# Kernel optimization log

Measured on AMD Instinct MI355X. Metric: run time of the kernel, lower is better.

## Reference

```python
import jax, jax.numpy as jnp
import numpy as np

WINDOW, STRIDE, BLUR_THR, EPS = 8, 4, 50.0, 1e-5
DN = ('NCHW', 'OIHW', 'NCHW')


def _conv(x, w, pad=0, stride=1):
    return jax.lax.conv_general_dilated(x, w, (stride, stride), [(pad, pad), (pad, pad)], dimension_numbers=DN)


def _detect_rgb_invalid(rgb):
    # Laplacian-variance blur detector: unfold(8,stride=4) -> var -> threshold -> scatter windows
    B, _, H, W = rgb.shape
    gray = 0.299 * rgb[:, 0] + 0.587 * rgb[:, 1] + 0.114 * rgb[:, 2]
    gray = jnp.clip(gray * 255.0, 0.0, 255.0)[:, None]  # [B,1,H,W]
    lap_k = jnp.array([[0., 1., 0.], [1., -4., 1.], [0., 1., 0.]], gray.dtype)[None, None]
    lap = _conv(gray, lap_k, pad=1)
    ones_k = jnp.ones((1, 1, WINDOW, WINDOW), gray.dtype)
    s1 = jax.lax.conv_general_dilated(lap, ones_k, (STRIDE, STRIDE), 'VALID', dimension_numbers=DN)
    s2 = jax.lax.conv_general_dilated(lap * lap, ones_k, (STRIDE, STRIDE), 'VALID', dimension_numbers=DN)
    n = float(WINDOW * WINDOW)
    var = (s2 - s1 * s1 / n) / (n - 1.0)  # unbiased var, matches torch.var
    flags = (var[:, 0] < BLUR_THR).astype(gray.dtype)  # [B, hs, ws]
    hs, ws = flags.shape[1], flags.shape[2]
    rep = jnp.repeat(jnp.repeat(flags, STRIDE, axis=1), STRIDE, axis=2)  # [B, hs*4, ws*4]
    mask = jnp.zeros((B, H, W), gray.dtype)
    # each 8x8 window covers 2x2 stride-cells -> max over the 4 shifted copies
    for dy in range(0, WINDOW, STRIDE):
        for dx in range(0, WINDOW, STRIDE):
            mask = mask.at[:, dy:dy + hs * STRIDE, dx:dx + ws * STRIDE].max(rep)
    return mask


def _bn_relu(x, g, b):
    m = x.mean((0, 2, 3), keepdims=True)
    v = x.var((0, 2, 3), keepdims=True)  # biased, matches BN training-mode normalization
    return jax.nn.relu(g[None, :, None, None] * (x - m) / jnp.sqrt(v + EPS) + b[None, :, None, None])


def _attend(main, aux, inv, ft_w, bn_g, bn_b, sa_w, ca1_w, ca2_w):
    B, C, H, W = main.shape
    aux_t = _bn_relu(_conv(aux, ft_w, pad=1), bn_g, bn_b)
    xs = jnp.broadcast_to(jnp.linspace(-1.0, 1.0, W, dtype=main.dtype)[None, None, None, :], (B, 1, H, W))
    ys = jnp.broadcast_to(jnp.linspace(-1.0, 1.0, H, dtype=main.dtype)[None, None, :, None], (B, 1, H, W))
    sp_in = jnp.concatenate([main.mean(1, keepdims=True), main.max(axis=1, keepdims=True), xs, ys], axis=1)
    sw = jax.nn.sigmoid(_conv(sp_in, sa_w, pad=3))  # [B,1,H,W]
    gap = main.mean((2, 3), keepdims=True)
    cw = jax.nn.sigmoid(_conv(jax.nn.relu(_conv(gap, ca1_w)), ca2_w))  # [B,C,1,1]
    return aux_t * sw * cw * (1.0 + inv[:, None])


def _compensate(main, aux, inv, params):
    # early-return when mask is all-zero in torch is mathematically identical to the blend
    comp = _attend(main, aux, inv, *params)
    m = inv[:, None]
    return main * (1.0 - m) + comp * m


def _down(mask, h, w):
    H, W = mask.shape[1], mask.shape[2]
    return mask[:, ::H // h, ::W // w]  # exact nearest-neighbor for integer ratios


def _forward(rgb_feat0, rgb_feat1, rgb_feat2, depth_feat0, depth_feat1, depth_feat2, rgb_img, depth_img,
             ft_w0, bn_g0, bn_b0, sa_w0, ca1_w0, ca2_w0,
             ft_w1, bn_g1, bn_b1, sa_w1, ca1_w1, ca2_w1,
             ft_w2, bn_g2, bn_b2, sa_w2, ca1_w2, ca2_w2):
    rgb_mask = _detect_rgb_invalid(rgb_img)
    depth_mask = (depth_img[:, 2] <= 0.0).astype(rgb_img.dtype)
    rgb_feats = (rgb_feat0, rgb_feat1, rgb_feat2)
    depth_feats = (depth_feat0, depth_feat1, depth_feat2)
    params = ((ft_w0, bn_g0, bn_b0, sa_w0, ca1_w0, ca2_w0),
              (ft_w1, bn_g1, bn_b1, sa_w1, ca1_w1, ca2_w1),
              (ft_w2, bn_g2, bn_b2, sa_w2, ca1_w2, ca2_w2))
    outs_r, outs_d = [], []
    for rf, df, p in zip(rgb_feats, depth_feats, params):
        h, w = rf.shape[2], rf.shape[3]
        ri = _down(rgb_mask, h, w)
        di = _down(depth_mask, h, w)
        outs_r.append(_compensate(rf, df, ri, p))
        outs_d.append(_compensate(df, rf, di, p))
    return tuple(outs_r) + tuple(outs_d)


def setup_inputs() -> dict:
    key = jax.random.key(0)
    ks = iter(jax.random.split(key, 40))
    B, H, W = 8, 512, 512
    chans = [256, 512, 1024]
    feat_hw = [(64, 64), (32, 32), (16, 16)]
    d = {}
    for i, (C, (fh, fw)) in enumerate(zip(chans, feat_hw)):
        d[f'rgb_feat{i}'] = jax.random.normal(next(ks), (B, C, fh, fw), jnp.float32)
        d[f'depth_feat{i}'] = jax.random.normal(next(ks), (B, C, fh, fw), jnp.float32)
    d['rgb_img'] = jax.random.uniform(next(ks), (B, 3, H, W), jnp.float32)
    d['depth_img'] = jax.random.normal(next(ks), (B, 3, H, W), jnp.float32)
    for i, C in enumerate(chans):
        r = C // 16
        d[f'ft_w{i}'] = jax.random.normal(next(ks), (C, C, 3, 3), jnp.float32) * 0.02
        d[f'bn_g{i}'] = jnp.ones((C,), jnp.float32)
        d[f'bn_b{i}'] = jnp.zeros((C,), jnp.float32)
        d[f'sa_w{i}'] = jax.random.normal(next(ks), (1, 4, 7, 7), jnp.float32) * 0.1
        d[f'ca1_w{i}'] = jax.random.normal(next(ks), (r, C, 1, 1), jnp.float32) * 0.1
        d[f'ca2_w{i}'] = jax.random.normal(next(ks), (C, r, 1, 1), jnp.float32) * 0.1
    return d


def reference(rgb_feat0, rgb_feat1, rgb_feat2, depth_feat0, depth_feat1, depth_feat2, rgb_img, depth_img,
              ft_w0, bn_g0, bn_b0, sa_w0, ca1_w0, ca2_w0,
              ft_w1, bn_g1, bn_b1, sa_w1, ca1_w1, ca2_w1,
              ft_w2, bn_g2, bn_b2, sa_w2, ca1_w2, ca2_w2):
    return _forward(rgb_feat0, rgb_feat1, rgb_feat2, depth_feat0, depth_feat1, depth_feat2, rgb_img, depth_img,
                    ft_w0, bn_g0, bn_b0, sa_w0, ca1_w0, ca2_w0,
                    ft_w1, bn_g1, bn_b1, sa_w1, ca1_w1, ca2_w1,
                    ft_w2, bn_g2, bn_b2, sa_w2, ca1_w2, ca2_w2)
```

## Files before the change

kernel.cpp:

```cpp
#include <hip/hip_runtime.h>
#include <math.h>

#define B8 8
typedef unsigned short ushort_t;
typedef __attribute__((ext_vector_type(8))) short bf16x8;
typedef __attribute__((ext_vector_type(4))) float f32x4;

static __device__ __forceinline__ float sigmoidf_(float x){ return 1.f/(1.f+expf(-x)); }

static __device__ __forceinline__ ushort_t f2bf(float f){
  unsigned u = __float_as_uint(f);
  u = u + 0x7fffu + ((u>>16)&1u);
  return (ushort_t)(u>>16);
}
static __device__ __forceinline__ float bflo(unsigned q){ return __uint_as_float(q << 16); }
static __device__ __forceinline__ float bfhi(unsigned q){ return __uint_as_float(q & 0xffff0000u); }

__device__ __forceinline__ void gload_lds16(const ushort_t* g, ushort_t* l){
  __builtin_amdgcn_global_load_lds((const __attribute__((address_space(1))) unsigned int*)(const void*)g,
                                   (__attribute__((address_space(3))) unsigned int*)(void*)l, 16, 0, 0);
}

__global__ __launch_bounds__(256) void k_flags2(const float* __restrict__ rgb,
                                                float* __restrict__ flags){
  __shared__ float sg[70][71];
  int bx = blockIdx.x & 7, by = (blockIdx.x >> 3) & 7, b = blockIdx.x >> 6;
  int wy0 = by*16, wx0 = bx*16;
  int y0 = 4*wy0 - 1, x0 = 4*wx0 - 1;
  const float* p = rgb + (size_t)b*3*262144;
  int tid = threadIdx.x;
  for (int i = tid; i < 70*70; i += 256){
    int r = i/70, cX = i%70;
    int y = y0 + r, x = x0 + cX;
    float v = 0.f;
    if (y>=0 && y<512 && x>=0 && x<512){
      int ii = y*512+x;
      v = 0.299f*p[ii] + 0.587f*p[ii+262144] + 0.114f*p[ii+524288];
      v = fminf(fmaxf(v*255.f, 0.f), 255.f);
    }
    sg[r][cX] = v;
  }
  __syncthreads();
  int wy = wy0 + (tid>>4), wx = wx0 + (tid&15);
  if (wy > 126 || wx > 126) return;
  int ry = 4*(tid>>4) + 1, rx = 4*(tid&15) + 1;
  float s1 = 0.f, s2 = 0.f;
  #pragma unroll
  for (int iy=0; iy<8; ++iy){
    int r = ry+iy;
    #pragma unroll
    for (int ix=0; ix<8; ++ix){
      int cX = rx+ix;
      float c = sg[r][cX];
      float lap = sg[r-1][cX] + sg[r+1][cX] + sg[r][cX-1] + sg[r][cX+1] - 4.f*c;
      s1 += lap; s2 += lap*lap;
    }
  }
  float var = (s2 - s1*s1*(1.f/64.f)) * (1.f/63.f);
  flags[(size_t)b*16129 + wy*127 + wx] = (var < 50.f) ? 1.f : 0.f;
}

__global__ void k_masks3(const float* __restrict__ flags, const float* __restrict__ depth,
                         float* __restrict__ ri0, float* __restrict__ di0,
                         float* __restrict__ ri1, float* __restrict__ di1,
                         float* __restrict__ ri2, float* __restrict__ di2){
  int idx = blockIdx.x*256 + threadIdx.x;
  const int n0 = 8*4096, n1 = 8*1024, n2 = 8*256;
  float* ri; float* di; int h, st, i2;
  if (idx < n0){ ri=ri0; di=di0; h=64; st=8;  i2=idx; }
  else if (idx < n0+n1){ ri=ri1; di=di1; h=32; st=16; i2=idx-n0; }
  else if (idx < n0+n1+n2){ ri=ri2; di=di2; h=16; st=32; i2=idx-n0-n1; }
  else return;
  int b = i2/(h*h), i = i2%(h*h);
  int y = (i/h)*st, x = (i%h)*st;
  const float* f = flags + (size_t)b*16129;
  int fy = y>>2, fx = x>>2;
  float v = f[fy*127+fx];
  if (y>0)         v = fmaxf(v, f[(fy-1)*127+fx]);
  if (x>0)         v = fmaxf(v, f[fy*127+fx-1]);
  if (y>0 && x>0)  v = fmaxf(v, f[(fy-1)*127+fx-1]);
  ri[i2] = v;
  const int IHW = 262144;
  di[i2] = (depth[(size_t)b*3*IHW + 2*IHW + (size_t)y*512 + x] <= 0.f) ? 1.f : 0.f;
}

template<int C>
__global__ __launch_bounds__(256) void k_wrd2(const float* __restrict__ w, ushort_t* __restrict__ outp){
  __shared__ float swp[9*C];
  int co = blockIdx.x, tid = threadIdx.x;
  const int n = 9*C;
  const float* src = w + (size_t)co*n;
  for (int i=tid;i<n;i+=256) swp[i]=src[i];
  __syncthreads();
  ushort_t* dst = outp + (size_t)co*n;
  for (int j=tid;j<n;j+=256){
    int cb  = j / 576;
    int rem = j - cb*576;
    int kq  = rem >> 6;
    int cin = rem & 63;
    dst[j] = f2bf(swp[(cb*64 + cin)*9 + kq]);
  }
}

template<int C, int H, int W>
__global__ __launch_bounds__(256) void k_prep(const float* __restrict__ rgbf,
                                              const float* __restrict__ depf,
                                              ushort_t* __restrict__ outp,
                                              float* __restrict__ gpart,
                                              float* __restrict__ pmean,
                                              float* __restrict__ pmax_){
  const int W2 = W+2, H2 = H+2, CB = C/64;
  const int NHSZ = B8*H2*W2*C;
  const int HW = H*W;
  __shared__ float st[64*66];
  __shared__ float red[4][64];
  int bi = blockIdx.x;
  int f  = bi & 1; bi >>= 1;
  int cb = bi % CB; bi /= CB;
  int yy = bi % H2;
  int b  = bi / H2;
  int tid = threadIdx.x;
  const float* in = (f==0) ? rgbf : depf;
  int ndir = f ^ 1;
  ushort_t* outrow = outp + (size_t)ndir*NHSZ + ((size_t)(b*H2 + yy)*W2)*C + cb*64;
  bool pad_row = (yy == 0) || (yy == H2-1);
  if (!pad_row){
    int y = yy-1;
    const float* src = in + ((size_t)(b*C + cb*64)*H + y)*W;
    for (int i=tid; i<64*W; i+=256){
      int c = i / W, x = i % W;
      st[x*66 + c] = src[(size_t)c*H*W + x];
    }
  }
  __syncthreads();
  for (int j=tid; j<W2*8; j+=256){
    int x = j >> 3, cc = (j & 7)*8;
    ushort_t tmp[8];
    if (pad_row || x == 0 || x == W2-1){
      #pragma unroll
      for (int q=0;q<8;++q) tmp[q]=0;
    } else {
      const float* sp = &st[(x-1)*66 + cc];
      float2 a0 = *(const float2*)(sp+0);
      float2 a1 = *(const float2*)(sp+2);
      float2 a2 = *(const float2*)(sp+4);
      float2 a3 = *(const float2*)(sp+6);
      tmp[0]=f2bf(a0.x); tmp[1]=f2bf(a0.y); tmp[2]=f2bf(a1.x); tmp[3]=f2bf(a1.y);
      tmp[4]=f2bf(a2.x); tmp[5]=f2bf(a2.y); tmp[6]=f2bf(a3.x); tmp[7]=f2bf(a3.y);
    }
    *(bf16x8*)&outrow[(size_t)x*C + cc] = *(bf16x8*)tmp;
  }
  if (pad_row) return;
  int y = yy - 1;
  {
    int c = tid & 63, quarter = tid >> 6;
    float s = 0.f;
    for (int x = quarter; x < W; x += 4) s += st[x*66 + c];
    red[quarter][c] = s;
  }
  if (tid < W*4){
    int x = tid >> 2, sl = tid & 3;
    float ps = 0.f, pmx = -INFINITY;
    #pragma unroll
    for (int k=0;k<16;++k){
      float v = st[x*66 + sl*16 + k];
      ps += v; pmx = fmaxf(pmx, v);
    }
    ps += __shfl_xor(ps, 1); pmx = fmaxf(pmx, __shfl_xor(pmx, 1));
    ps += __shfl_xor(ps, 2); pmx = fmaxf(pmx, __shfl_xor(pmx, 2));
    if (sl == 0){
      size_t po = ((size_t)f*CB + cb)*((size_t)B8*HW) + (size_t)b*HW + (size_t)y*W + x;
      pmean[po] = ps; pmax_[po] = pmx;
    }
  }
  __syncthreads();
  if (tid < 64){
    float t4 = red[0][tid]+red[1][tid]+red[2][tid]+red[3][tid];
    gpart[(((size_t)f*B8 + b)*H + y)*C + (size_t)cb*64 + tid] = t4;
  }
}

template<int C, int H, int W, int KS>
__global__ __launch_bounds__(512)
void k_gemm_conv(const ushort_t* __restrict__ Aw, const ushort_t* __restrict__ nh,
                 ushort_t* __restrict__ Gm){
  const int K9 = 9*C;
  const int HW = H*W;
  const int N  = B8*HW;
  const int H2 = H+2, W2 = W+2;
  const int NT_N = N/256, NT_M = C/256;
  const int KCT = 36;
  const int NHSZ = B8*H2*W2*C;
  __shared__ ushort_t sA[2][16384];
  __shared__ ushort_t sB[2][16384];
  int tid = threadIdx.x;

  const int nwg = 2*KS*NT_M*NT_N;
  const int MK  = 2*KS*NT_M;
  int bid = blockIdx.x;
  int swz = (bid & 7)*(nwg >> 3) + (bid >> 3);
  int mk  = swz % MK;
  int n_t = swz / MK;
  int m_t = mk % NT_M;
  int kz2 = mk / NT_M;
  int dir = kz2 / KS, kz = kz2 % KS;

  const ushort_t* nhd = nh + (size_t)dir*NHSZ;
  int m0 = m_t*256, n0 = n_t*256;
  int l = tid & 63, wv_id = tid >> 6;
  int wm = wv_id >> 2, wn = wv_id & 3;
  int lrow = l & 15, lq = l >> 4;
  int lx7 = lrow & 7;

  long long aoffA[2][2], boffB[2][2];
  #pragma unroll
  for (int h=0; h<2; ++h){
    #pragma unroll
    for (int j=0; j<2; ++j){
      int c = j*512 + tid;
      int lr = h*128 + (c>>3);
      int slot = c & 7;
      int lslot = slot ^ (lr & 7);
      int q_ = lr >> 6, wm_ = (lr>>5)&1, loc = lr & 31;
      int r = wm_*128 + q_*32 + loc;
      aoffA[h][j] = (long long)(m0 + r)*K9 + lslot*8;
      int nn = n0 + lr;
      int b_ = nn / HW, rhw = nn % HW;
      int y = rhw / W, x = rhw % W;
      boffB[h][j] = ((long long)(b_*H2 + y + 1)*W2 + (x + 1))*(long long)C + lslot*8;
    }
  }

#define STAGE_A(s_, h_, kc_) do{                                    \
    long long oK = (long long)(kc_) << 6;                           \
    ushort_t* d0 = &sA[s_][(h_)*8192 + tid*8];                      \
    gload_lds16(Aw + aoffA[h_][0] + oK, d0);                        \
    gload_lds16(Aw + aoffA[h_][1] + oK, d0 + 4096);                 \
  }while(0)
#define STAGE_B(s_, h_, kc_) do{                                    \
    int cb_ = (kc_)/9, kq_ = (kc_) - cb_*9;                         \
    long long dv = (long long)((kq_/3 - 1)*W2 + (kq_%3 - 1))*C + ((long long)cb_<<6); \
    ushort_t* d0 = &sB[s_][(h_)*8192 + tid*8];                      \
    gload_lds16(nhd + boffB[h_][0] + dv, d0);                       \
    gload_lds16(nhd + boffB[h_][1] + dv, d0 + 4096);                \
  }while(0)

  f32x4 acc[8][4];
  #pragma unroll
  for (int i=0;i<8;++i)
    #pragma unroll
    for (int j=0;j<4;++j) acc[i][j] = (f32x4){0.f,0.f,0.f,0.f};

  int kc0 = kz*KCT;

  STAGE_A(0,0,kc0);   STAGE_A(0,1,kc0);
  STAGE_B(0,0,kc0);   STAGE_B(0,1,kc0);
  STAGE_B(1,0,kc0+1); STAGE_B(1,1,kc0+1);
  STAGE_A(1,0,kc0+1);
  asm volatile("s_waitcnt vmcnt(6)" ::: "memory");
  __builtin_amdgcn_s_barrier();

  for (int t=0; t<KCT; ++t){
    int cur = t & 1, nxt = cur ^ 1;
    int kc = kc0 + t;
    bf16x8 bf[4][2], afA[2][2], afB[2][2];

    #pragma unroll
    for (int ni=0;ni<4;++ni)
      #pragma unroll
      for (int kk=0;kk<2;++kk)
        bf[ni][kk] = *(const bf16x8*)&sB[cur][(wn*64 + ni*16 + lrow)*64 + ((kk*4+lq)^lx7)*8];
    #pragma unroll
    for (int mi=0;mi<2;++mi)
      #pragma unroll
      for (int kk=0;kk<2;++kk)
        afA[mi][kk] = *(const bf16x8*)&sA[cur][(wm*32 + mi*16 + lrow)*64 + ((kk*4+lq)^lx7)*8];
    #pragma unroll
    for (int mi=0;mi<2;++mi)
      #pragma unroll
      for (int kk=0;kk<2;++kk)
        afB[mi][kk] = *(const bf16x8*)&sA[cur][(64 + wm*32 + mi*16 + lrow)*64 + ((kk*4+lq)^lx7)*8];
    if (t+1 < KCT) STAGE_A(nxt,1,kc+1);
    __builtin_amdgcn_s_setprio(1);
    #pragma unroll
    for (int kk=0;kk<2;++kk)
      #pragma unroll
      for (int mi=0;mi<2;++mi)
        #pragma unroll
        for (int ni=0;ni<4;++ni)
          acc[mi][ni] = __builtin_amdgcn_mfma_f32_16x16x32_bf16(afA[mi][kk], bf[ni][kk], acc[mi][ni], 0,0,0);
    __builtin_amdgcn_s_setprio(0);
    asm volatile("s_waitcnt lgkmcnt(0)" ::: "memory");
    __builtin_amdgcn_sched_barrier(0);
    __builtin_amdgcn_s_barrier();

    #pragma unroll
    for (int mi=0;mi<2;++mi)
      #pragma unroll
      for (int kk=0;kk<2;++kk)
        afA[mi][kk] = *(const bf16x8*)&sA[cur][(128 + wm*32 + mi*16 + lrow)*64 + ((kk*4+lq)^lx7)*8];
    if (t+2 < KCT) STAGE_B(cur,0,kc+2);
    __builtin_amdgcn_s_setprio(1);
    #pragma unroll
    for (int kk=0;kk<2;++kk)
      #pragma unroll
      for (int mi=0;mi<2;++mi)
        #pragma unroll
        for (int ni=0;ni<4;++ni)
          acc[2+mi][ni] = __builtin_amdgcn_mfma_f32_16x16x32_bf16(afB[mi][kk], bf[ni][kk], acc[2+mi][ni], 0,0,0);
    __builtin_amdgcn_s_setprio(0);

    #pragma unroll
    for (int mi=0;mi<2;++mi)
      #pragma unroll
      for (int kk=0;kk<2;++kk)
        afB[mi][kk] = *(const bf16x8*)&sA[cur][(192 + wm*32 + mi*16 + lrow)*64 + ((kk*4+lq)^lx7)*8];
    if (t+2 < KCT) STAGE_B(cur,1,kc+2);
    __builtin_amdgcn_s_setprio(1);
    #pragma unroll
    for (int kk=0;kk<2;++kk)
      #pragma unroll
      for (int mi=0;mi<2;++mi)
        #pragma unroll
        for (int ni=0;ni<4;++ni)
          acc[4+mi][ni] = __builtin_amdgcn_mfma_f32_16x16x32_bf16(afA[mi][kk], bf[ni][kk], acc[4+mi][ni], 0,0,0);
    __builtin_amdgcn_s_setprio(0);

    if (t+2 < KCT) STAGE_A(cur,0,kc+2);
    __builtin_amdgcn_s_setprio(1);
    #pragma unroll
    for (int kk=0;kk<2;++kk)
      #pragma unroll
      for (int mi=0;mi<2;++mi)
        #pragma unroll
        for (int ni=0;ni<4;++ni)
          acc[6+mi][ni] = __builtin_amdgcn_mfma_f32_16x16x32_bf16(afB[mi][kk], bf[ni][kk], acc[6+mi][ni], 0,0,0);
    __builtin_amdgcn_s_setprio(0);
    if (t+2 < KCT) { asm volatile("s_waitcnt vmcnt(6)" ::: "memory"); }
    else           { asm volatile("s_waitcnt vmcnt(0)" ::: "memory"); }
    __builtin_amdgcn_sched_barrier(0);
    __builtin_amdgcn_s_barrier();
  }
#undef STAGE_A
#undef STAGE_B

  ushort_t* po = Gm + (size_t)kz2*C*N;
  #pragma unroll
  for (int ai=0;ai<8;++ai)
    #pragma unroll
    for (int ni=0;ni<4;++ni)
      #pragma unroll
      for (int r=0;r<4;++r)
        po[(size_t)(m0 + wm*128 + ai*16 + lq*4 + r)*N + n0 + wn*64 + ni*16 + lrow] = f2bf(acc[ai][ni][r]);
}

__global__ void k_sgc(const float* __restrict__ pmean, const float* __restrict__ pmax_,
                      float* __restrict__ spmean, float* __restrict__ spmax,
                      int CG, int BHW, float invC){
  int dir = blockIdx.y;
  int p = blockIdx.x*256 + threadIdx.x;
  if (p >= BHW) return;
  const float* pm = pmean + (size_t)dir*CG*BHW;
  const float* px = pmax_ + (size_t)dir*CG*BHW;
  float s = 0.f, m = -INFINITY;
  for (int g=0; g<CG; ++g){
    s += pm[(size_t)g*BHW + p];
    m = fmaxf(m, px[(size_t)g*BHW + p]);
  }
  spmean[(size_t)dir*BHW + p] = s*invC;
  spmax [(size_t)dir*BHW + p] = m;
}

__global__ void k_sw(const float* __restrict__ spmean, const float* __restrict__ spmax,
                     const float* __restrict__ sa, float* __restrict__ sw,
                     int H, int W){
  __shared__ float s_sa[196];
  int tid = threadIdx.x;
  if (tid < 196) s_sa[tid] = sa[tid];
  __syncthreads();
  int HW = H*W;
  int dir = blockIdx.y;
  int gpos = blockIdx.x*256 + tid;
  if (gpos >= B8*HW) return;
  int b = gpos/HW, i = gpos%HW;
  int y = i/W, x = i%W;
  float inv_w = 2.f/(float)(W-1), inv_h = 2.f/(float)(H-1);
  const float* pm = spmean + (size_t)dir*B8*HW + (size_t)b*HW;
  const float* px = spmax  + (size_t)dir*B8*HW + (size_t)b*HW;
  float acc = 0.f;
  for (int ky=0;ky<7;++ky){
    int yy = y+ky-3;
    if (yy<0 || yy>=H) continue;
    float ysv = -1.f + yy*inv_h;
    for (int kx=0;kx<7;++kx){
      int xx = x+kx-3;
      if (xx<0 || xx>=W) continue;
      float xsv = -1.f + xx*inv_w;
      int kk = ky*7+kx;
      acc += s_sa[kk]*pm[yy*W+xx] + s_sa[49+kk]*px[yy*W+xx]
           + s_sa[98+kk]*xsv + s_sa[147+kk]*ysv;
    }
  }
  sw[(size_t)dir*B8*HW + gpos] = sigmoidf_(acc);
}

__global__ void k_mlp(const float* __restrict__ gpart, const float* __restrict__ w1,
                      const float* __restrict__ w2, float* __restrict__ cw,
                      int C, int R, int SPLIT, float invHW){
  int b = blockIdx.x, dir = blockIdx.y;
  int tid = threadIdx.x;
  __shared__ float sg[1024];
  __shared__ float sh[64];
  const float* gp = gpart + (((size_t)dir*B8 + b)*SPLIT)*C;
  for (int c=tid;c<C;c+=256){
    float s = 0.f;
    for (int sp=0; sp<SPLIT; ++sp) s += gp[(size_t)sp*C + c];
    sg[c] = s*invHW;
  }
  __syncthreads();
  int r = tid>>2, q = tid&3;
  if (r < R){
    float s = 0.f;
    for (int c=q;c<C;c+=4) s += w1[(size_t)r*C + c]*sg[c];
    s += __shfl_xor(s,1); s += __shfl_xor(s,2);
    if (q==0) sh[r] = fmaxf(s, 0.f);
  }
  __syncthreads();
  for (int c2=tid; c2<C; c2+=256){
    float s = 0.f;
    for (int rr=0;rr<R;++rr) s += w2[(size_t)c2*R + rr]*sh[rr];
    cw[(size_t)dir*B8*C + (size_t)b*C + c2] = sigmoidf_(s);
  }
}

__global__ __launch_bounds__(256)
void k_bnfinal(const float* __restrict__ rgbf, const float* __restrict__ depf,
               const ushort_t* __restrict__ G,
               const float* __restrict__ g, const float* __restrict__ bb,
               const float* __restrict__ swp, const float* __restrict__ cwp,
               const float* __restrict__ ri, const float* __restrict__ di,
               float* __restrict__ out_r, float* __restrict__ out_d,
               int C, int HW, int hwShift, int ks){
  extern __shared__ char bnf_smem[];
  int c = blockIdx.x, dir = blockIdx.y, tid = threadIdx.x;
  int N = B8*HW;
  size_t MN = (size_t)C*N;
  const ushort_t* p0 = G + (size_t)dir*ks*MN + (size_t)c*N;
  const float* main_ = (dir==0) ? rgbf : depf;
  const float* mask  = (dir==0) ? ri : di;
  float* out = (dir==0) ? out_r : out_d;

  float s1 = 0.f, s2 = 0.f;
  if (ks == 1){
    uint4* cache = (uint4*)bnf_smem;
    for (int i = tid*8; i < N; i += 2048){
      uint4 q = *(const uint4*)(p0 + i);
      cache[i>>3] = q;
      float v0=bflo(q.x), v1=bfhi(q.x), v2=bflo(q.y), v3=bfhi(q.y);
      float v4=bflo(q.z), v5=bfhi(q.z), v6=bflo(q.w), v7=bfhi(q.w);
      s1 += v0+v1+v2+v3+v4+v5+v6+v7;
      s2 += v0*v0+v1*v1+v2*v2+v3*v3+v4*v4+v5*v5+v6*v6+v7*v7;
    }
  } else {
    float* cache = (float*)bnf_smem;
    for (int i = tid*8; i < N; i += 2048){
      float v[8];
      #pragma unroll
      for (int q=0;q<8;++q) v[q]=0.f;
      for (int kz=0; kz<ks; ++kz){
        uint4 q = *(const uint4*)(p0 + (size_t)kz*MN + i);
        v[0]+=bflo(q.x); v[1]+=bfhi(q.x); v[2]+=bflo(q.y); v[3]+=bfhi(q.y);
        v[4]+=bflo(q.z); v[5]+=bfhi(q.z); v[6]+=bflo(q.w); v[7]+=bfhi(q.w);
      }
      #pragma unroll
      for (int q=0;q<8;++q){ cache[i+q] = v[q]; s1 += v[q]; s2 += v[q]*v[q]; }
    }
  }
  __shared__ float sb1[4], sb2[4];
  __shared__ float sab[2];
  #pragma unroll
  for (int off=32; off; off>>=1){ s1 += __shfl_down(s1,off); s2 += __shfl_down(s2,off); }
  int wid = tid>>6;
  if ((tid&63)==0){ sb1[wid]=s1; sb2[wid]=s2; }
  __syncthreads();
  if (tid==0){
    float t1 = sb1[0]+sb1[1]+sb1[2]+sb1[3];
    float t2 = sb2[0]+sb2[1]+sb2[2]+sb2[3];
    float Nf = (float)N;
    float mean = t1/Nf;
    float var  = t2/Nf - mean*mean;
    float a = g[c] / sqrtf(var + 1e-5f);
    sab[0] = a;
    sab[1] = bb[c] - mean*a;
  }
  __syncthreads();
  float a = sab[0], bta = sab[1];

  for (int i = tid*8; i < N; i += 2048){
    float v[8];
    if (ks == 1){
      uint4 q = ((const uint4*)bnf_smem)[i>>3];
      v[0]=bflo(q.x); v[1]=bfhi(q.x); v[2]=bflo(q.y); v[3]=bfhi(q.y);
      v[4]=bflo(q.z); v[5]=bfhi(q.z); v[6]=bflo(q.w); v[7]=bfhi(q.w);
    } else {
      #pragma unroll
      for (int q=0;q<8;++q) v[q] = ((const float*)bnf_smem)[i+q];
    }
    int b  = i >> hwShift;
    int hw = i - (b << hwShift);
    const float* mkp = mask + (size_t)b*HW + hw;
    const float* mnp = main_ + ((size_t)b*C + c)*HW + hw;
    const float* swq = swp + (size_t)dir*B8*HW + (size_t)b*HW + hw;
    float cwv = 2.f * cwp[(size_t)dir*B8*C + (size_t)b*C + c];
    float4 mk0 = *(const float4*)(mkp),   mk1 = *(const float4*)(mkp+4);
    float4 mn0 = *(const float4*)(mnp),   mn1 = *(const float4*)(mnp+4);
    float4 sw0 = *(const float4*)(swq),   sw1 = *(const float4*)(swq+4);
    float4 o0, o1;
    o0.x = (mk0.x > 0.5f) ? fmaxf(a*v[0] + bta, 0.f)*sw0.x*cwv : mn0.x;
    o0.y = (mk0.y > 0.5f) ? fmaxf(a*v[1] + bta, 0.f)*sw0.y*cwv : mn0.y;
    o0.z = (mk0.z > 0.5f) ? fmaxf(a*v[2] + bta, 0.f)*sw0.z*cwv : mn0.z;
    o0.w = (mk0.w > 0.5f) ? fmaxf(a*v[3] + bta, 0.f)*sw0.w*cwv : mn0.w;
    o1.x = (mk1.x > 0.5f) ? fmaxf(a*v[4] + bta, 0.f)*sw1.x*cwv : mn1.x;
    o1.y = (mk1.y > 0.5f) ? fmaxf(a*v[5] + bta, 0.f)*sw1.y*cwv : mn1.y;
    o1.z = (mk1.z > 0.5f) ? fmaxf(a*v[6] + bta, 0.f)*sw1.z*cwv : mn1.z;
    o1.w = (mk1.w > 0.5f) ? fmaxf(a*v[7] + bta, 0.f)*sw1.w*cwv : mn1.w;
    float* op = out + ((size_t)b*C + c)*HW + hw;
    *(float4*)(op)   = o0;
    *(float4*)(op+4) = o1;
  }
}

extern "C" void kernel_launch(void* const* d_in, const int* in_sizes, int n_in,
                              void* d_out, int out_size, void* d_ws, size_t ws_size,
                              hipStream_t stream){
  (void)in_sizes; (void)n_in; (void)out_size; (void)ws_size;
  const int B = B8;
  const float* rgb_feat[3] = {(const float*)d_in[0], (const float*)d_in[2], (const float*)d_in[4]};
  const float* dep_feat[3] = {(const float*)d_in[1], (const float*)d_in[3], (const float*)d_in[5]};
  const float* rgb_img = (const float*)d_in[6];
  const float* dep_img = (const float*)d_in[7];

  const int Cs[3]   = {256, 512, 1024};
  const int hs[3]   = {64, 32, 16};
  const int HWs[3]  = {64*64, 32*32, 16*16};
  const int KSs[3]  = {1, 2, 4};
  const int HWSH[3] = {12, 10, 8};
  const unsigned BNSM[3] = {65536, 32768, 8192};

  float* ws = (float*)d_ws;
  ushort_t* Gm = (ushort_t*)ws;
  float* flags = ws;
  float* rdbase = ws + 8388608;
  float* ri[3]; float* di[3];
  {
    size_t o = 0;
    for (int s=0;s<3;++s){
      ri[s] = rdbase + o; o += (size_t)B*hs[s]*hs[s];
      di[s] = rdbase + o; o += (size_t)B*hs[s]*hs[s];
    }
  }
  float* SB = rdbase + 86016;
  float* ST = SB + 9220096;
  float* swb    = ST + 0;
  float* gpart  = ST + 65536;
  float* cwb    = ST + 327680;
  float* spmean = ST + 344064;
  float* spmax  = ST + 409600;
  float* pmeanp = ST + 475136;
  float* pmaxp  = ST + 737280;

  k_flags2<<<512, 256, 0, stream>>>(rgb_img, flags);
  k_masks3<<<168, 256, 0, stream>>>(flags, dep_img, ri[0], di[0], ri[1], di[1], ri[2], di[2]);

  const size_t outoff_r[3] = {0,         8388608u,  12582912u};
  const size_t outoff_d[3] = {14680064u, 23068672u, 27262976u};
  float* outp = (float*)d_out;

  for (int s=0;s<3;++s){
    const float* ftw = (const float*)d_in[8 +6*s];
    const float* bng = (const float*)d_in[9 +6*s];
    const float* bnb = (const float*)d_in[10+6*s];
    const float* saw = (const float*)d_in[11+6*s];
    const float* ca1 = (const float*)d_in[12+6*s];
    const float* ca2 = (const float*)d_in[13+6*s];
    int C = Cs[s], HW = HWs[s], h = hs[s];
    int R = C/16;
    int BHW = B*HW;
    int ks = KSs[s];

    size_t nh_f = (size_t)B*(h+2)*(h+2)*C;
    ushort_t* nhbf = (ushort_t*)SB;
    ushort_t* wbf  = (ushort_t*)(SB + nh_f);

    if (s==0) k_wrd2<256> <<<256,  256, 0, stream>>>(ftw, wbf);
    if (s==1) k_wrd2<512> <<<512,  256, 0, stream>>>(ftw, wbf);
    if (s==2) k_wrd2<1024><<<1024, 256, 0, stream>>>(ftw, wbf);

    {
      unsigned nb = (unsigned)(B*(h+2)*(C/64)*2);
      if (s==0) k_prep<256, 64,64><<<nb, 256, 0, stream>>>(rgb_feat[s], dep_feat[s], nhbf, gpart, pmeanp, pmaxp);
      if (s==1) k_prep<512, 32,32><<<nb, 256, 0, stream>>>(rgb_feat[s], dep_feat[s], nhbf, gpart, pmeanp, pmaxp);
      if (s==2) k_prep<1024,16,16><<<nb, 256, 0, stream>>>(rgb_feat[s], dep_feat[s], nhbf, gpart, pmeanp, pmaxp);
    }

    if (s==0) k_gemm_conv<256, 64,64,1><<<256, 512, 0, stream>>>(wbf, nhbf, Gm);
    if (s==1) k_gemm_conv<512, 32,32,2><<<256, 512, 0, stream>>>(wbf, nhbf, Gm);
    if (s==2) k_gemm_conv<1024,16,16,4><<<256, 512, 0, stream>>>(wbf, nhbf, Gm);

    k_sgc<<<dim3((BHW+255)/256,2), 256, 0, stream>>>(pmeanp, pmaxp, spmean, spmax, C/64, BHW, 1.f/(float)C);
    k_sw <<<dim3((B*HW+255)/256,2), 256, 0, stream>>>(spmean, spmax, saw, swb, h, h);
    k_mlp<<<dim3(B,2), 256, 0, stream>>>(gpart, ca1, ca2, cwb, C, R, hs[s], 1.f/(float)HW);

    k_bnfinal<<<dim3(C,2), 256, BNSM[s], stream>>>(
        rgb_feat[s], dep_feat[s], Gm, bng, bnb, swb, cwb,
        ri[s], di[s], outp + outoff_r[s], outp + outoff_d[s], C, HW, HWSH[s], ks);
  }
}
```

Baseline: 518.8 us.

## Fuse channel-group reduction, spatial attention conv, and channel MLP into one kernel

Replaces three small per-scale kernels (group reduction of partial mean/max, 7x7 spatial attention conv, channel-attention MLP) with a single templated kernel. Spatial blocks reduce the partial sums for a row band plus halo into shared memory and apply the 7x7 conv from there. Extra blocks in the same grid handle the MLP. This removes two launches per scale and the global round-trip of the intermediate spmean/spmax buffers, at the cost of recomputing halo rows and running few blocks at the smallest scale.

```diff
diff --git a/kernel.cpp b/kernel.cpp
--- a/kernel.cpp
+++ b/kernel.cpp
@@ -354,82 +354,91 @@
         po[(size_t)(m0 + wm*128 + ai*16 + lq*4 + r)*N + n0 + wn*64 + ni*16 + lrow] = f2bf(acc[ai][ni][r]);
 }
 
-__global__ void k_sgc(const float* __restrict__ pmean, const float* __restrict__ pmax_,
-                      float* __restrict__ spmean, float* __restrict__ spmax,
-                      int CG, int BHW, float invC){
-  int dir = blockIdx.y;
-  int p = blockIdx.x*256 + threadIdx.x;
-  if (p >= BHW) return;
-  const float* pm = pmean + (size_t)dir*CG*BHW;
-  const float* px = pmax_ + (size_t)dir*CG*BHW;
-  float s = 0.f, m = -INFINITY;
-  for (int g=0; g<CG; ++g){
-    s += pm[(size_t)g*BHW + p];
-    m = fmaxf(m, px[(size_t)g*BHW + p]);
-  }
-  spmean[(size_t)dir*BHW + p] = s*invC;
-  spmax [(size_t)dir*BHW + p] = m;
-}
-
-__global__ void k_sw(const float* __restrict__ spmean, const float* __restrict__ spmax,
-                     const float* __restrict__ sa, float* __restrict__ sw,
-                     int H, int W){
+template<int C, int H, int R>
+__global__ __launch_bounds__(256) void k_att(const float* __restrict__ pmean,
+                                             const float* __restrict__ pmax_,
+                                             const float* __restrict__ gpart,
+                                             const float* __restrict__ sa,
+                                             const float* __restrict__ w1,
+                                             const float* __restrict__ w2,
+                                             float* __restrict__ sw,
+                                             float* __restrict__ cw,
+                                             int Rr, float invHW){
+  const int CG = C/64;
+  const int HW = H*H;
+  const int swB = B8*(H/R);
   __shared__ float s_sa[196];
-  int tid = threadIdx.x;
-  if (tid < 196) s_sa[tid] = sa[tid];
-  __syncthreads();
-  int HW = H*W;
-  int dir = blockIdx.y;
-  int gpos = blockIdx.x*256 + tid;
-  if (gpos >= B8*HW) return;
-  int b = gpos/HW, i = gpos%HW;
-  int y = i/W, x = i%W;
-  float inv_w = 2.f/(float)(W-1), inv_h = 2.f/(float)(H-1);
-  const float* pm = spmean + (size_t)dir*B8*HW + (size_t)b*HW;
-  const float* px = spmax  + (size_t)dir*B8*HW + (size_t)b*HW;
-  float acc = 0.f;
-  for (int ky=0;ky<7;++ky){
-    int yy = y+ky-3;
-    if (yy<0 || yy>=H) continue;
-    float ysv = -1.f + yy*inv_h;
-    for (int kx=0;kx<7;++kx){
-      int xx = x+kx-3;
-      if (xx<0 || xx>=W) continue;
-      float xsv = -1.f + xx*inv_w;
-      int kk = ky*7+kx;
-      acc += s_sa[kk]*pm[yy*W+xx] + s_sa[49+kk]*px[yy*W+xx]
-           + s_sa[98+kk]*xsv + s_sa[147+kk]*ysv;
-    }
-  }
-  sw[(size_t)dir*B8*HW + gpos] = sigmoidf_(acc);
-}
-
-__global__ void k_mlp(const float* __restrict__ gpart, const float* __restrict__ w1,
-                      const float* __restrict__ w2, float* __restrict__ cw,
-                      int C, int R, int SPLIT, float invHW){
-  int b = blockIdx.x, dir = blockIdx.y;
-  int tid = threadIdx.x;
+  __shared__ float spm[(R+6)*H];
+  __shared__ float spx[(R+6)*H];
   __shared__ float sg[1024];
   __shared__ float sh[64];
-  const float* gp = gpart + (((size_t)dir*B8 + b)*SPLIT)*C;
-  for (int c=tid;c<C;c+=256){
-    float s = 0.f;
-    for (int sp=0; sp<SPLIT; ++sp) s += gp[(size_t)sp*C + c];
-    sg[c] = s*invHW;
-  }
-  __syncthreads();
-  int r = tid>>2, q = tid&3;
-  if (r < R){
-    float s = 0.f;
-    for (int c=q;c<C;c+=4) s += w1[(size_t)r*C + c]*sg[c];
-    s += __shfl_xor(s,1); s += __shfl_xor(s,2);
-    if (q==0) sh[r] = fmaxf(s, 0.f);
-  }
-  __syncthreads();
-  for (int c2=tid; c2<C; c2+=256){
-    float s = 0.f;
-    for (int rr=0;rr<R;++rr) s += w2[(size_t)c2*R + rr]*sh[rr];
-    cw[(size_t)dir*B8*C + (size_t)b*C + c2] = sigmoidf_(s);
+  int dir = blockIdx.y;
+  int bx = blockIdx.x;
+  int tid = threadIdx.x;
+  float invC = 1.f/(float)C;
+
+  if (bx < swB){
+    if (tid < 196) s_sa[tid] = sa[tid];
+    int b = bx / (H/R), rb = bx % (H/R);
+    int y0 = rb*R;
+    for (int i = tid; i < (R+6)*H; i += 256){
+      int y = y0 - 3 + i/H;
+      int x = i % H;
+      float s = 0.f, m = -INFINITY;
+      if (y >= 0 && y < H){
+        #pragma unroll
+        for (int g=0; g<CG; ++g){
+          size_t po = ((size_t)dir*CG + g)*((size_t)B8*HW) + (size_t)b*HW + (size_t)y*H + x;
+          s += pmean[po];
+          m = fmaxf(m, pmax_[po]);
+        }
+      }
+      spm[i] = s*invC;
+      spx[i] = m;
+    }
+    __syncthreads();
+    int x = tid % H, yl = tid / H;
+    int y = y0 + yl;
+    float inv_w = 2.f/(float)(H-1);
+    float acc = 0.f;
+    for (int ky=0;ky<7;++ky){
+      int gy = y+ky-3;
+      if (gy<0 || gy>=H) continue;
+      float ysv = -1.f + gy*inv_w;
+      int lr = yl + ky;
+      for (int kx=0;kx<7;++kx){
+        int gx = x+kx-3;
+        if (gx<0 || gx>=H) continue;
+        float xsv = -1.f + gx*inv_w;
+        int kk = ky*7+kx;
+        acc += s_sa[kk]*spm[lr*H+gx] + s_sa[49+kk]*spx[lr*H+gx]
+             + s_sa[98+kk]*xsv + s_sa[147+kk]*ysv;
+      }
+    }
+    sw[(size_t)dir*B8*HW + (size_t)b*HW + (size_t)y*H + x] = sigmoidf_(acc);
+  } else {
+    int b = bx - swB;
+    int Rch = C/16;
+    const float* gp = gpart + (((size_t)dir*B8 + b)*H)*C;
+    for (int c=tid;c<C;c+=256){
+      float s = 0.f;
+      for (int sp=0; sp<H; ++sp) s += gp[(size_t)sp*C + c];
+      sg[c] = s*invHW;
+    }
+    __syncthreads();
+    int r = tid>>2, q = tid&3;
+    if (r < Rch){
+      float s = 0.f;
+      for (int c=q;c<C;c+=4) s += w1[(size_t)r*C + c]*sg[c];
+      s += __shfl_xor(s,1); s += __shfl_xor(s,2);
+      if (q==0) sh[r] = fmaxf(s, 0.f);
+    }
+    __syncthreads();
+    for (int c2=tid; c2<C; c2+=256){
+      float s = 0.f;
+      for (int rr=0;rr<Rch;++rr) s += w2[(size_t)c2*Rch + rr]*sh[rr];
+      cw[(size_t)dir*B8*C + (size_t)b*C + c2] = sigmoidf_(s);
+    }
   }
 }
 
@@ -564,10 +573,8 @@
   float* swb    = ST + 0;
   float* gpart  = ST + 65536;
   float* cwb    = ST + 327680;
-  float* spmean = ST + 344064;
-  float* spmax  = ST + 409600;
-  float* pmeanp = ST + 475136;
-  float* pmaxp  = ST + 737280;
+  float* pmeanp = ST + 344064;
+  float* pmaxp  = ST + 606208;
 
   k_flags2<<<512, 256, 0, stream>>>(rgb_img, flags);
   k_masks3<<<168, 256, 0, stream>>>(flags, dep_img, ri[0], di[0], ri[1], di[1], ri[2], di[2]);
@@ -584,7 +591,6 @@
     const float* ca1 = (const float*)d_in[12+6*s];
     const float* ca2 = (const float*)d_in[13+6*s];
     int C = Cs[s], HW = HWs[s], h = hs[s];
-    int R = C/16;
     int BHW = B*HW;
     int ks = KSs[s];
 
@@ -607,9 +613,12 @@
     if (s==1) k_gemm_conv<512, 32,32,2><<<256, 512, 0, stream>>>(wbf, nhbf, Gm);
     if (s==2) k_gemm_conv<1024,16,16,4><<<256, 512, 0, stream>>>(wbf, nhbf, Gm);
 
-    k_sgc<<<dim3((BHW+255)/256,2), 256, 0, stream>>>(pmeanp, pmaxp, spmean, spmax, C/64, BHW, 1.f/(float)C);
-    k_sw <<<dim3((B*HW+255)/256,2), 256, 0, stream>>>(spmean, spmax, saw, swb, h, h);
-    k_mlp<<<dim3(B,2), 256, 0, stream>>>(gpart, ca1, ca2, cwb, C, R, hs[s], 1.f/(float)HW);
+    {
+      float invHW = 1.f/(float)HW;
+      if (s==0) k_att<256, 64, 4><<<dim3((unsigned)(B*16 + B),2), 256, 0, stream>>>(pmeanp, pmaxp, gpart, saw, ca1, ca2, swb, cwb, 0, invHW);
+      if (s==1) k_att<512, 32, 8><<<dim3((unsigned)(B*4  + B),2), 256, 0, stream>>>(pmeanp, pmaxp, gpart, saw, ca1, ca2, swb, cwb, 0, invHW);
+      if (s==2) k_att<1024,16,16><<<dim3((unsigned)(B*1  + B),2), 256, 0, stream>>>(pmeanp, pmaxp, gpart, saw, ca1, ca2, swb, cwb, 0, invHW);
+    }
 
     k_bnfinal<<<dim3(C,2), 256, BNSM[s], stream>>>(
         rgb_feat[s], dep_feat[s], Gm, bng, bnb, swb, cwb,
```

Result: faster. 454.7 us (median of 2 runs) (-12.4%).
